# Kernel tuning notes

Hardware: AMD Instinct MI355X
Metric: run time of the kernel (lower is better)

## Reference

```python
import jax, jax.numpy as jnp
import numpy as np

B, T, D, H, O = 256, 512, 128, 128, 64


def setup_inputs() -> dict:
    key = jax.random.key(0)
    ks = jax.random.split(key, 10)
    s = 1.0 / np.sqrt(H)
    u = lambda k, shape: jax.random.uniform(k, shape, jnp.float32, -s, s)
    return {
        "x": jax.random.normal(ks[0], (B, T, D), jnp.float32),
        "W_ih": u(ks[1], (4 * H, D)),   # torch gate order: i, f, g, o
        "W_hh": u(ks[2], (4 * H, H)),
        "b_ih": u(ks[3], (4 * H,)),
        "b_hh": u(ks[4], (4 * H,)),
        "W1": u(ks[5], (H, H)),
        "b1": u(ks[6], (H,)),
        "W2": u(ks[7], (O, H)),
        "b2": u(ks[8], (O,)),
    }


def lstm_scan(x, W_ih, W_hh, b_ih, b_hh):
    b, t, _ = x.shape
    h4 = W_hh.shape[0] // 4
    # precompute input contribution for all timesteps (one big GEMM)
    xg = jnp.einsum('btd,gd->btg', x, W_ih) + b_ih + b_hh  # (B,T,4H)
    xg = jnp.swapaxes(xg, 0, 1)  # (T,B,4H) for scan over time

    def step(carry, xg_t):
        h, c = carry
        g = xg_t + h @ W_hh.T  # (B,4H)
        i, f, gg, o = jnp.split(g, 4, axis=-1)
        i = jax.nn.sigmoid(i)
        f = jax.nn.sigmoid(f)
        gg = jnp.tanh(gg)
        o = jax.nn.sigmoid(o)
        c = f * c + i * gg
        h = o * jnp.tanh(c)
        return (h, c), h

    h0 = jnp.zeros((b, h4), x.dtype)
    c0 = jnp.zeros((b, h4), x.dtype)
    _, hs = jax.lax.scan(step, (h0, c0), xg)  # hs: (T,B,H)
    return jnp.swapaxes(hs, 0, 1)  # (B,T,H), matching torch batch_first


def reference(x, W_ih, W_hh, b_ih, b_hh, W1, b1, W2, b2):
    b, t, _ = x.shape
    h = lstm_scan(x, W_ih, W_hh, b_ih, b_hh)          # (B,T,H)
    hflat = h.reshape(-1, h.shape[-1])                 # (B*T,H), b-major (as torch)
    hflat = hflat @ W1.T + b1
    y = hflat @ W2.T + b2                              # (B*T,O)
    # faithful to original: reshape flattened b-major rows as (T,B,O), take [-1]
    y = y.reshape(t, b, -1)
    return y[-1]                                       # (B,O)
```

## Files before the change

### kernel.cpp

```cpp
#include <hip/hip_runtime.h>
#include <math.h>

#define BB 256
#define TT 512
#define DD 128
#define HH 128
#define GG 512
#define OO 64

typedef _Float16 half8 __attribute__((ext_vector_type(8)));
typedef float    f32x4 __attribute__((ext_vector_type(4)));

__device__ __forceinline__ float sigmoid_fast(float x) {
    return __builtin_amdgcn_rcpf(1.0f + __expf(-x));
}
__device__ __forceinline__ float tanh_fast(float x) {
    float e = __expf(2.0f * fabsf(x));
    float t = fmaf(-2.0f, __builtin_amdgcn_rcpf(e + 1.0f), 1.0f);
    return copysignf(t, x);
}

__global__ __launch_bounds__(512) void xgpack_kernel(
    const float* __restrict__ x,
    const float* __restrict__ W_ih,
    const float* __restrict__ b_ih,
    const float* __restrict__ b_hh,
    const float* __restrict__ W_hh,
    float* __restrict__ xg,
    _Float16* __restrict__ Wp)
{
    if (blockIdx.x >= TT) {
        const int g = (blockIdx.x - TT) * 512 + threadIdx.x;
        const int fid = g >> 6, l = g & 63;
        const int w = fid >> 5, rem = fid & 31, nt = rem >> 2, kt = rem & 3;
        const int quad = l >> 4, col = l & 15;
        const int row = (nt >> 1) * 128 + (nt & 1) * 16 + w * 32 + col;
        const int off = kt * 32 + quad * 8;
        const float* s = W_hh + row * HH + off;
        _Float16* d = Wp + (size_t)g * 8;
#pragma unroll
        for (int i = 0; i < 8; i++) d[i] = (_Float16)s[i];
        return;
    }

    const int t = blockIdx.x;
    const int g = threadIdx.x;

    __shared__ __align__(16) float xs[DD];
    if (g < DD) xs[g] = x[(255 * TT + t) * DD + g];
    __syncthreads();

    const float4* __restrict__ wrow = (const float4*)(W_ih + g * DD);
    const float4* __restrict__ xv   = (const float4*)xs;

    float a0 = 0.f, a1 = 0.f, a2 = 0.f, a3 = 0.f;
#pragma unroll
    for (int i = 0; i < DD / 4; i += 4) {
        float4 w0 = wrow[i + 0], w1 = wrow[i + 1], w2 = wrow[i + 2], w3 = wrow[i + 3];
        float4 h0 = xv[i + 0],  h1 = xv[i + 1],  h2 = xv[i + 2],  h3 = xv[i + 3];
        a0 += w0.x * h0.x + w0.y * h0.y + w0.z * h0.z + w0.w * h0.w;
        a1 += w1.x * h1.x + w1.y * h1.y + w1.z * h1.z + w1.w * h1.w;
        a2 += w2.x * h2.x + w2.y * h2.y + w2.z * h2.z + w2.w * h2.w;
        a3 += w3.x * h3.x + w3.y * h3.y + w3.z * h3.z + w3.w * h3.w;
    }
    const float val = (a0 + a1) + (a2 + a3) + b_ih[g] + b_hh[g];
    xg[t * GG + (g & 127) * 4 + (g >> 7)] = val;
}

__global__
__attribute__((amdgpu_flat_work_group_size(256, 256), amdgpu_waves_per_eu(1, 1)))
void scan_kernel(
    const _Float16* __restrict__ Wp,
    const float* __restrict__ xgp,
    float* __restrict__ hs)
{
    const int tid  = threadIdx.x;
    const int lane = tid & 63;
    const int w    = tid >> 6;
    const int col  = lane & 15;
    const int quad = lane >> 4;
    const int wbase = w * 32;
    const bool sel  = (lane >= 32);
    const int jsel  = wbase + (sel ? 16 : 0) + col;
    const int aoff  = quad * 8;
    const bool wr   = (quad == 0) || (quad == 3);

    __shared__ __align__(16) _Float16 h_lds[2][HH];

#define BLOADP(nt, kt) \
    half8 B##nt##_##kt = *(const half8*)(Wp + (((w * 32 + (nt) * 4 + (kt)) * 64 + lane) * 8));
#define FOR_KT(X, nt) X(nt, 0) X(nt, 1) X(nt, 2) X(nt, 3)
#define FOR_NT(X) FOR_KT(X, 0) FOR_KT(X, 1) FOR_KT(X, 2) FOR_KT(X, 3) \
                  FOR_KT(X, 4) FOR_KT(X, 5) FOR_KT(X, 6) FOR_KT(X, 7)
    FOR_NT(BLOADP)

    asm volatile("" : "+v"(B0_0), "+v"(B0_1), "+v"(B0_2), "+v"(B0_3),
                      "+v"(B1_0), "+v"(B1_1), "+v"(B1_2), "+v"(B1_3),
                      "+v"(B2_0), "+v"(B2_1), "+v"(B2_2), "+v"(B2_3),
                      "+v"(B3_0), "+v"(B3_1), "+v"(B3_2), "+v"(B3_3));
    asm volatile("" : "+v"(B4_0), "+v"(B4_1), "+v"(B4_2), "+v"(B4_3),
                      "+v"(B5_0), "+v"(B5_1), "+v"(B5_2), "+v"(B5_3),
                      "+v"(B6_0), "+v"(B6_1), "+v"(B6_2), "+v"(B6_3),
                      "+v"(B7_0), "+v"(B7_1), "+v"(B7_2), "+v"(B7_3));

    if (tid < HH) h_lds[0][tid] = (_Float16)0.f;

    f32x4 Z = {0.f, 0.f, 0.f, 0.f};
    asm volatile("" : "+v"(Z));

    const float* __restrict__ xgl = xgp + jsel * 4;
    f32x4 xg0 = *(const f32x4*)(xgl + 0 * GG);
    f32x4 xg1 = *(const f32x4*)(xgl + 1 * GG);

    float c = 0.f;
    __syncthreads();

#define MM(a, b, cc) __builtin_amdgcn_mfma_f32_16x16x32_f16((a), (b), (cc), 0, 0, 0)
#define STEP(par, XCUR) do {                                                            \
    const int t = t2 + (par);                                                           \
    f32x4 xpf = *(const f32x4*)(xgl + ((t + 2) & (TT - 1)) * GG);                       \
    const _Float16* hl = h_lds[(par)];                                                  \
    half8 A0 = *(const half8*)(hl +  0 + aoff);                                         \
    half8 A1 = *(const half8*)(hl + 32 + aoff);                                         \
    half8 A2 = *(const half8*)(hl + 64 + aoff);                                         \
    half8 A3 = *(const half8*)(hl + 96 + aoff);                                         \
    f32x4 C0, C1, C2, C3, C4, C5, C6, C7;                                               \
    C4 = MM(A0, B4_0, Z);  C5 = MM(A0, B5_0, Z);  C0 = MM(A0, B0_0, Z);                 \
    C1 = MM(A0, B1_0, Z);  C2 = MM(A0, B2_0, Z);  C3 = MM(A0, B3_0, Z);                 \
    C6 = MM(A0, B6_0, Z);  C7 = MM(A0, B7_0, Z);                                        \
    C4 = MM(A1, B4_1, C4); C5 = MM(A1, B5_1, C5); C0 = MM(A1, B0_1, C0);                \
    C1 = MM(A1, B1_1, C1); C2 = MM(A1, B2_1, C2); C3 = MM(A1, B3_1, C3);                \
    C6 = MM(A1, B6_1, C6); C7 = MM(A1, B7_1, C7);                                       \
    C4 = MM(A2, B4_2, C4); C5 = MM(A2, B5_2, C5); C0 = MM(A2, B0_2, C0);                \
    C1 = MM(A2, B1_2, C1); C2 = MM(A2, B2_2, C2); C3 = MM(A2, B3_2, C3);                \
    C6 = MM(A2, B6_2, C6); C7 = MM(A2, B7_2, C7);                                       \
    C4 = MM(A3, B4_3, C4); C5 = MM(A3, B5_3, C5); C0 = MM(A3, B0_3, C0);                \
    C1 = MM(A3, B1_3, C1); C2 = MM(A3, B2_3, C2); C3 = MM(A3, B3_3, C3);                \
    C6 = MM(A3, B6_3, C6); C7 = MM(A3, B7_3, C7);                                       \
    float pg = (sel ? C5[0] : C4[0]) + (XCUR).z;                                        \
    float pi = (sel ? C1[0] : C0[0]) + (XCUR).x;                                        \
    float pf = (sel ? C3[0] : C2[0]) + (XCUR).y;                                        \
    float po = (sel ? C7[0] : C6[0]) + (XCUR).w;                                        \
    float gv = tanh_fast(pg);                                                           \
    float iv = sigmoid_fast(pi);                                                        \
    float fv = sigmoid_fast(pf);                                                        \
    c = fv * c + iv * gv;                                                               \
    float ov = sigmoid_fast(po);                                                        \
    float hval = ov * tanh_fast(c);                                                     \
    if (wr) {                                                                           \
        h_lds[1 - (par)][jsel] = (_Float16)hval;                                        \
        hs[(t & (BB - 1)) * HH + jsel] = hval;       \
    }                                                                                   \
    asm volatile("s_waitcnt lgkmcnt(0)\n\ts_barrier" ::: "memory");                     \
    (XCUR) = xpf;                                                                       \
} while (0)

    for (int t2 = 0; t2 < TT; t2 += 2) {
        STEP(0, xg0);
        STEP(1, xg1);
    }
#undef STEP
#undef MM
}

__global__ __launch_bounds__(128) void mlp_kernel(
    const float* __restrict__ hs,
    const float* __restrict__ W1,
    const float* __restrict__ b1,
    const float* __restrict__ W2,
    const float* __restrict__ b2,
    float* __restrict__ out)
{
    const int r = blockIdx.x;
    const int j = threadIdx.x;

    __shared__ __align__(16) float hsh[HH];
    __shared__ __align__(16) float z[HH];

    hsh[j] = hs[r * HH + j];
    __syncthreads();

    {
        const float4* __restrict__ wrow = (const float4*)(W1 + j * HH);
        const float4* __restrict__ hv   = (const float4*)hsh;
        float acc = b1[j];
#pragma unroll
        for (int i = 0; i < 32; i++) {
            float4 ww = wrow[i], h = hv[i];
            acc += ww.x * h.x + ww.y * h.y + ww.z * h.z + ww.w * h.w;
        }
        z[j] = acc;
    }
    __syncthreads();

    if (j < OO) {
        const float4* __restrict__ wrow = (const float4*)(W2 + j * HH);
        const float4* __restrict__ zv   = (const float4*)z;
        float acc = b2[j];
#pragma unroll
        for (int i = 0; i < 32; i++) {
            float4 ww = wrow[i], zz = zv[i];
            acc += ww.x * zz.x + ww.y * zz.y + ww.z * zz.z + ww.w * zz.w;
        }
        out[r * OO + j] = acc;
    }
}

extern "C" void kernel_launch(void* const* d_in, const int* in_sizes, int n_in,
                              void* d_out, int out_size, void* d_ws, size_t ws_size,
                              hipStream_t stream) {
    const float* x    = (const float*)d_in[0];
    const float* W_ih = (const float*)d_in[1];
    const float* W_hh = (const float*)d_in[2];
    const float* b_ih = (const float*)d_in[3];
    const float* b_hh = (const float*)d_in[4];
    const float* W1   = (const float*)d_in[5];
    const float* b1   = (const float*)d_in[6];
    const float* W2   = (const float*)d_in[7];
    const float* b2   = (const float*)d_in[8];
    float* out = (float*)d_out;

    float*    xg = (float*)d_ws;
    float*    hs = xg + TT * GG;
    _Float16* Wp = (_Float16*)(hs + BB * HH);

    xgpack_kernel<<<TT + 16, 512, 0, stream>>>(x, W_ih, b_ih, b_hh, W_hh, xg, Wp);
    scan_kernel<<<1, 256, 0, stream>>>(Wp, xg, hs);
    mlp_kernel<<<BB, 128, 0, stream>>>(hs, W1, b1, W2, b2, out);
}
```

Measured before the change: 347.1 us.

## Prescale gate weights by log2e and split activations across lane pairs via swizzle

Folds the log2(e) factors (and 2·log2(e) for the g gate) into the packed W_hh and into the precomputed input gates, so the recurrent step can call exp2 directly without extra multiplies. The four gate activations are divided between quad pairs: even quads compute the i and f sigmoids, odd quads compute tanh(g) and the o sigmoid. A ds_swizzle then exchanges the results so every lane holds all four. The cell state is kept scaled by 2·log2(e), which lets the final tanh use exp2 directly and shortens the serial per-step critical path. In exchange it adds swizzle latency, and rounding the prescaled weights to fp16 may shift numerics slightly.

```diff
diff --git a/kernel.cpp b/kernel.cpp
--- a/kernel.cpp
+++ b/kernel.cpp
@@ -8,16 +8,16 @@
 #define GG 512
 #define OO 64
 
+#define LOG2E    1.44269504088896340736f
+#define TWOLOG2E 2.88539008177792681472f
+
 typedef _Float16 half8 __attribute__((ext_vector_type(8)));
 typedef float    f32x4 __attribute__((ext_vector_type(4)));
 
-__device__ __forceinline__ float sigmoid_fast(float x) {
-    return __builtin_amdgcn_rcpf(1.0f + __expf(-x));
-}
-__device__ __forceinline__ float tanh_fast(float x) {
-    float e = __expf(2.0f * fabsf(x));
-    float t = fmaf(-2.0f, __builtin_amdgcn_rcpf(e + 1.0f), 1.0f);
-    return copysignf(t, x);
+__device__ __forceinline__ float swz16(float v) {
+    int i = __builtin_bit_cast(int, v);
+    i = __builtin_amdgcn_ds_swizzle(i, 0x401F);
+    return __builtin_bit_cast(float, i);
 }
 
 __global__ __launch_bounds__(512) void xgpack_kernel(
@@ -36,10 +36,11 @@
         const int quad = l >> 4, col = l & 15;
         const int row = (nt >> 1) * 128 + (nt & 1) * 16 + w * 32 + col;
         const int off = kt * 32 + quad * 8;
+        const float ws = ((row >> 7) == 2) ? TWOLOG2E : LOG2E;
         const float* s = W_hh + row * HH + off;
         _Float16* d = Wp + (size_t)g * 8;
 #pragma unroll
-        for (int i = 0; i < 8; i++) d[i] = (_Float16)s[i];
+        for (int i = 0; i < 8; i++) d[i] = (_Float16)(s[i] * ws);
         return;
     }
 
@@ -63,7 +64,8 @@
         a2 += w2.x * h2.x + w2.y * h2.y + w2.z * h2.z + w2.w * h2.w;
         a3 += w3.x * h3.x + w3.y * h3.y + w3.z * h3.z + w3.w * h3.w;
     }
-    const float val = (a0 + a1) + (a2 + a3) + b_ih[g] + b_hh[g];
+    const float scale = ((g >> 7) == 2) ? TWOLOG2E : LOG2E;
+    const float val = ((a0 + a1) + (a2 + a3) + b_ih[g] + b_hh[g]) * scale;
     xg[t * GG + (g & 127) * 4 + (g >> 7)] = val;
 }
 
@@ -81,6 +83,7 @@
     const int quad = lane >> 4;
     const int wbase = w * 32;
     const bool sel  = (lane >= 32);
+    const bool odd  = (quad & 1);
     const int jsel  = wbase + (sel ? 16 : 0) + col;
     const int aoff  = quad * 8;
     const bool wr   = (quad == 0) || (quad == 3);
@@ -137,16 +140,32 @@
     C4 = MM(A3, B4_3, C4); C5 = MM(A3, B5_3, C5); C0 = MM(A3, B0_3, C0);                \
     C1 = MM(A3, B1_3, C1); C2 = MM(A3, B2_3, C2); C3 = MM(A3, B3_3, C3);                \
     C6 = MM(A3, B6_3, C6); C7 = MM(A3, B7_3, C7);                                       \
-    float pg = (sel ? C5[0] : C4[0]) + (XCUR).z;                                        \
+                   \
     float pi = (sel ? C1[0] : C0[0]) + (XCUR).x;                                        \
     float pf = (sel ? C3[0] : C2[0]) + (XCUR).y;                                        \
+    float pg = (sel ? C5[0] : C4[0]) + (XCUR).z;                                        \
     float po = (sel ? C7[0] : C6[0]) + (XCUR).w;                                        \
-    float gv = tanh_fast(pg);                                                           \
-    float iv = sigmoid_fast(pi);                                                        \
-    float fv = sigmoid_fast(pf);                                                        \
-    c = fv * c + iv * gv;                                                               \
-    float ov = sigmoid_fast(po);                                                        \
-    float hval = ov * tanh_fast(c);                                                     \
+                             \
+    float pa = odd ? pg : pi;                                                           \
+    float pb = odd ? po : pf;                                                           \
+    float ax = odd ? fabsf(pa) : -pa;                                                   \
+    float ea = __builtin_amdgcn_exp2f(ax);                                              \
+    float ra = __builtin_amdgcn_rcpf(1.0f + ea);                                        \
+    float T  = copysignf(TWOLOG2E, pa);                                                 \
+    float va = odd ? fmaf(-2.0f * T, ra, T) : ra;       \
+    float eb = __builtin_amdgcn_exp2f(-pb);                                             \
+    float vb = __builtin_amdgcn_rcpf(1.0f + eb);                 \
+    float sa = swz16(va);                                                               \
+    float sb = swz16(vb);                                                               \
+    float iv  = odd ? sa : va;                                                          \
+    float gvs = odd ? va : sa;                                                          \
+    float fv  = odd ? sb : vb;                                                          \
+    float ov  = odd ? vb : sb;                                                          \
+    c = fmaf(fv, c, iv * gvs);                      \
+    float Ec = __builtin_amdgcn_exp2f(fabsf(c));                                        \
+    float rc = __builtin_amdgcn_rcpf(Ec + 1.0f);                                        \
+    float Ao = copysignf(ov, c);                                                        \
+    float hval = fmaf(-2.0f * Ao, rc, Ao);                                              \
     if (wr) {                                                                           \
         h_lds[1 - (par)][jsel] = (_Float16)hval;                                        \
         hs[(t & (BB - 1)) * HH + jsel] = hval;       \
```

After: 390.3 us. 12.5% more time.
